# Optimization experiments

Measured on AMD Instinct MI355X. Metric: run time of the kernel, lower is better.

## Reference

```python
import jax, jax.numpy as jnp
import numpy as np

D_MODEL = 1024
NUM_HEADS = 16
HEAD_DIM = D_MODEL // NUM_HEADS


def setup_inputs() -> dict:
    key = jax.random.key(0)
    ks = jax.random.split(key, 10)
    B, SQ, SKV = 4, 2048, 2048
    s = 1.0 / np.sqrt(D_MODEL)
    return {
        "query": jax.random.normal(ks[0], (B, SQ, D_MODEL), jnp.float32),
        "key_value": jax.random.normal(ks[1], (B, SKV, D_MODEL), jnp.float32),
        "Wq": jax.random.normal(ks[2], (D_MODEL, D_MODEL), jnp.float32) * s,
        "bq": jnp.zeros((D_MODEL,), jnp.float32),
        "Wk": jax.random.normal(ks[3], (D_MODEL, D_MODEL), jnp.float32) * s,
        "bk": jnp.zeros((D_MODEL,), jnp.float32),
        "Wv": jax.random.normal(ks[4], (D_MODEL, D_MODEL), jnp.float32) * s,
        "bv": jnp.zeros((D_MODEL,), jnp.float32),
        "Wo": jax.random.normal(ks[5], (D_MODEL, D_MODEL), jnp.float32) * s,
        "bo": jnp.zeros((D_MODEL,), jnp.float32),
    }


def reference(query, key_value, Wq, bq, Wk, bk, Wv, bv, Wo, bo):
    B, SQ, _ = query.shape
    SKV = key_value.shape[1]
    H, Dh = NUM_HEADS, HEAD_DIM
    # projections (torch Linear: x @ W.T + b); split heads -> (B, H, S, Dh)
    Q = (query @ Wq.T + bq).reshape(B, SQ, H, Dh).transpose(0, 2, 1, 3)
    K = (key_value @ Wk.T + bk).reshape(B, SKV, H, Dh).transpose(0, 2, 1, 3)
    V = (key_value @ Wv.T + bv).reshape(B, SKV, H, Dh).transpose(0, 2, 1, 3)
    scale = jnp.asarray(np.sqrt(Dh), query.dtype)
    scores = jnp.einsum("bhqd,bhkd->bhqk", Q, K) / scale
    weights = jax.nn.softmax(scores, axis=-1)  # dropout is identity in eval
    attn = jnp.einsum("bhqk,bhkd->bhqd", weights, V)
    attn = attn.transpose(0, 2, 1, 3).reshape(B, SQ, H * Dh)
    return attn @ Wo.T + bo
```

## Files before the change

### kernel.cpp

```cpp
#include <hip/hip_runtime.h>

#define NH 16
#define DH 64
#define DM 1024
#define SEQ 2048
#define BATCH 4

typedef short s16x8 __attribute__((ext_vector_type(8)));
typedef float f32x4 __attribute__((ext_vector_type(4)));

__device__ __forceinline__ unsigned short f2bf(float f) {
  union { float f; unsigned int u; } v; v.f = f;
  unsigned int u = v.u;
  unsigned int r = (u + 0x7fffu + ((u >> 16) & 1u)) >> 16;
  return (unsigned short)r;
}

__device__ __forceinline__ unsigned int pkbf(float a, float b) {
#if __has_builtin(__builtin_amdgcn_cvt_pk_bf16_f32)
  typedef short v2s __attribute__((ext_vector_type(2)));
  v2s r = __builtin_amdgcn_cvt_pk_bf16_f32(a, b);
  union { v2s v; unsigned int u; } cv; cv.v = r;
  return cv.u;
#else
  return (unsigned int)f2bf(a) | ((unsigned int)f2bf(b) << 16);
#endif
}

__device__ __forceinline__ float fexp2(float x) {
#if __has_builtin(__builtin_amdgcn_exp2f)
  return __builtin_amdgcn_exp2f(x);
#else
  return exp2f(x);
#endif
}

__device__ __forceinline__ void gload_lds16(const void* g, void* l) {
  __builtin_amdgcn_global_load_lds(
      (const __attribute__((address_space(1))) unsigned int*)g,
      (__attribute__((address_space(3))) unsigned int*)l, 16, 0, 0);
}

__global__ void convert_all(const float* __restrict__ q, const float* __restrict__ kv,
                            const float* __restrict__ w0, const float* __restrict__ w1,
                            const float* __restrict__ w2, const float* __restrict__ w3,
                            unsigned short* __restrict__ oq, unsigned short* __restrict__ okv,
                            unsigned short* __restrict__ ow0, unsigned short* __restrict__ ow1,
                            unsigned short* __restrict__ ow2, unsigned short* __restrict__ ow3) {
  const int NQ4 = (BATCH * SEQ * DM) / 4;
  const int NW4 = (DM * DM) / 4;
  const int total = NQ4 * 2 + NW4 * 4;
  for (int i = blockIdx.x * blockDim.x + threadIdx.x; i < total;
       i += gridDim.x * blockDim.x) {
    const float* s; unsigned short* d; int off;
    if (i < NQ4)            { s = q;  d = oq;  off = i; }
    else if (i < 2 * NQ4)   { s = kv; d = okv; off = i - NQ4; }
    else {
      int j = i - 2 * NQ4; int wsel = j / NW4; off = j - wsel * NW4;
      s = (wsel == 0) ? w0 : (wsel == 1) ? w1 : (wsel == 2) ? w2 : w3;
      d = (wsel == 0) ? ow0 : (wsel == 1) ? ow1 : (wsel == 2) ? ow2 : ow3;
    }
    float4 v = *(const float4*)(s + (size_t)off * 4);
    ushort4 o;
    o.x = f2bf(v.x); o.y = f2bf(v.y); o.z = f2bf(v.z); o.w = f2bf(v.w);
    *(ushort4*)(d + (size_t)off * 4) = o;
  }
}

__device__ __forceinline__ void gemm_tile(const unsigned short* __restrict__ X,
                                          const unsigned short* __restrict__ Wt,
                                          unsigned short* As, unsigned short* Bs,
                                          int m0, int n0, f32x4 (*acc)[4]) {
  const int tid = threadIdx.x;
  const int wv_ = tid >> 6, lane = tid & 63;
  const int quad = lane >> 4, c = lane & 15;
  const int wm = (wv_ >> 1) * 64, wn = (wv_ & 1) * 64;
  const int srow = lane >> 3;
  const int scol = ((lane & 7) ^ srow) * 8;

  for (int kt = 0; kt < DM; kt += 64) {
#pragma unroll
    for (int i = 0; i < 4; ++i) {
      int reg = wv_ * 4 + i;
      gload_lds16(X + (size_t)(m0 + reg * 8 + srow) * DM + kt + scol,
                  (void*)(As + reg * 512));
      gload_lds16(Wt + (size_t)(n0 + reg * 8 + srow) * DM + kt + scol,
                  (void*)(Bs + reg * 512));
    }
    __syncthreads();
#pragma unroll
    for (int k2 = 0; k2 < 2; ++k2) {
      s16x8 a[4], b[4];
      int g = k2 * 4 + quad;
#pragma unroll
      for (int t = 0; t < 4; ++t)
        a[t] = *(const s16x8*)(As + (wm + t * 16 + c) * 64 + ((g ^ (c & 7)) * 8));
#pragma unroll
      for (int t = 0; t < 4; ++t)
        b[t] = *(const s16x8*)(Bs + (wn + t * 16 + c) * 64 + ((g ^ (c & 7)) * 8));
#pragma unroll
      for (int tm = 0; tm < 4; ++tm)
#pragma unroll
        for (int tn = 0; tn < 4; ++tn)
          acc[tm][tn] = __builtin_amdgcn_mfma_f32_16x16x32_bf16(
              a[tm], b[tn], acc[tm][tn], 0, 0, 0);
    }
    __syncthreads();
  }
}

__global__ __launch_bounds__(256)
void gemm_qkv(const unsigned short* __restrict__ Xq,
              const unsigned short* __restrict__ Xkv,
              const unsigned short* __restrict__ W0,
              const unsigned short* __restrict__ W1,
              const unsigned short* __restrict__ W2,
              const float* __restrict__ b0, const float* __restrict__ b1,
              const float* __restrict__ b2,
              unsigned short* __restrict__ OQ, unsigned short* __restrict__ OK_,
              unsigned short* __restrict__ OV) {
  __shared__ alignas(16) unsigned short As[128 * 64];
  __shared__ alignas(16) unsigned short Bs[128 * 64];
  const int m0 = blockIdx.x * 128;
  const int ysel = blockIdx.y >> 3;
  const int n0 = (blockIdx.y & 7) * 128;
  const unsigned short* X = (ysel == 0) ? Xq : Xkv;
  const unsigned short* Wt = (ysel == 0) ? W0 : (ysel == 1) ? W1 : W2;
  const float* bias = (ysel == 0) ? b0 : (ysel == 1) ? b1 : b2;
  unsigned short* Out = (ysel == 0) ? OQ : (ysel == 1) ? OK_ : OV;
  const float scale = (ysel == 0) ? 0.1803368801f : 1.0f;

  f32x4 acc[4][4] = {};
  gemm_tile(X, Wt, As, Bs, m0, n0, acc);

  const int tid = threadIdx.x;
  const int wv_ = tid >> 6, lane = tid & 63;
  const int quad = lane >> 4, c = lane & 15;
  const int wm = (wv_ >> 1) * 64, wn = (wv_ & 1) * 64;
#pragma unroll
  for (int tm = 0; tm < 4; ++tm) {
#pragma unroll
    for (int tn = 0; tn < 4; ++tn) {
      int n = n0 + wn + tn * 16 + c;
      float bv = bias[n];
      int m_base = m0 + wm + tm * 16 + quad * 4;
      if (ysel == 2) {
        int b_ = m_base >> 11, s_ = m_base & 2047, h_ = n >> 6, dh = n & 63;
        size_t idx = (((size_t)(b_ * NH + h_)) * DH + dh) * SEQ + s_;
        ushort4 o4;
        o4.x = f2bf(acc[tm][tn][0] + bv);
        o4.y = f2bf(acc[tm][tn][1] + bv);
        o4.z = f2bf(acc[tm][tn][2] + bv);
        o4.w = f2bf(acc[tm][tn][3] + bv);
        *(ushort4*)(&Out[idx]) = o4;
      } else {
#pragma unroll
        for (int p = 0; p < 4; ++p) {
          int m = m_base + p;
          float val = (acc[tm][tn][p] + bv) * scale;
          int b_ = m >> 11, s_ = m & 2047, h_ = n >> 6, dh = n & 63;
          size_t idx = (((size_t)(b_ * NH + h_)) * SEQ + s_) * DH + dh;
          Out[idx] = f2bf(val);
        }
      }
    }
  }
}

__global__ __launch_bounds__(256)
void gemm_o(const unsigned short* __restrict__ X,
            const unsigned short* __restrict__ Wt,
            const float* __restrict__ bias, float* __restrict__ Out) {
  __shared__ alignas(16) unsigned short As[128 * 64];
  __shared__ alignas(16) unsigned short Bs[128 * 64];
  const int m0 = blockIdx.x * 128;
  const int n0 = blockIdx.y * 128;
  f32x4 acc[4][4] = {};
  gemm_tile(X, Wt, As, Bs, m0, n0, acc);

  const int tid = threadIdx.x;
  const int wv_ = tid >> 6, lane = tid & 63;
  const int quad = lane >> 4, c = lane & 15;
  const int wm = (wv_ >> 1) * 64, wn = (wv_ & 1) * 64;
#pragma unroll
  for (int tm = 0; tm < 4; ++tm) {
#pragma unroll
    for (int tn = 0; tn < 4; ++tn) {
      int n = n0 + wn + tn * 16 + c;
      float bv = bias[n];
#pragma unroll
      for (int p = 0; p < 4; ++p) {
        int m = m0 + wm + tm * 16 + quad * 4 + p;
        Out[(size_t)m * DM + n] = acc[tm][tn][p] + bv;
      }
    }
  }
}

__global__ __launch_bounds__(256, 4)
void attn_kernel(const unsigned short* __restrict__ Qb,
                 const unsigned short* __restrict__ Kb,
                 const unsigned short* __restrict__ VTb,
                 unsigned short* __restrict__ Ob) {
  __shared__ alignas(16) unsigned short SM[16384];

  const int tid = threadIdx.x, wv_ = tid >> 6, lane = tid & 63;
  const int quad = lane >> 4, c = lane & 15;
  const int bh = blockIdx.x, qb = blockIdx.y;
  const unsigned short* Qp = Qb + (size_t)bh * SEQ * DH;
  const unsigned short* Kp = Kb + (size_t)bh * SEQ * DH;
  const unsigned short* Vp = VTb + (size_t)bh * DH * SEQ;
  const int wq0 = qb * 128 + wv_ * 32;

  s16x8 aq[2][2];
#pragma unroll
  for (int t = 0; t < 2; ++t)
#pragma unroll
    for (int k2 = 0; k2 < 2; ++k2)
      aq[t][k2] = *(const s16x8*)(Qp + (size_t)(wq0 + t * 16 + c) * DH +
                                  k2 * 32 + quad * 8);

  f32x4 ot[4][2] = {};
  float lsum[2] = {};

  const int srow = lane >> 3;
  const int schunk = (lane & 7) ^ srow;

#pragma unroll
  for (int i = 0; i < 2; ++i) {
    int reg = wv_ * 2 + i;
    gload_lds16(Kp + (size_t)(reg * 8 + srow) * DH + schunk * 8,
                (void*)(SM + reg * 512));
    gload_lds16(Vp + (size_t)(reg * 8 + srow) * SEQ + schunk * 8,
                (void*)(SM + 8192 + reg * 512));
  }

  for (int kt = 0; kt < SEQ; kt += 64) {
    const int cur = (kt >> 6) & 1;
    __syncthreads();
    if (kt + 64 < SEQ) {
      const int nxt = cur ^ 1;
#pragma unroll
      for (int i = 0; i < 2; ++i) {
        int reg = wv_ * 2 + i;
        gload_lds16(Kp + (size_t)(kt + 64 + reg * 8 + srow) * DH + schunk * 8,
                    (void*)(SM + nxt * 4096 + reg * 512));
        gload_lds16(Vp + (size_t)(reg * 8 + srow) * SEQ + kt + 64 + schunk * 8,
                    (void*)(SM + 8192 + nxt * 4096 + reg * 512));
      }
    }
    const unsigned short* K_ = SM + cur * 4096;
    const unsigned short* V_ = SM + 8192 + cur * 4096;

    f32x4 s[2][2][2] = {};
#pragma unroll
    for (int k2 = 0; k2 < 2; ++k2) {
      s16x8 ak[2][2];
#pragma unroll
      for (int jp = 0; jp < 2; ++jp)
#pragma unroll
        for (int h = 0; h < 2; ++h) {
          int r = jp * 32 + ((c >> 2) << 3) + h * 4 + (c & 3);
          int g = k2 * 4 + quad;
          ak[jp][h] = *(const s16x8*)(K_ + r * 64 + ((g ^ (r & 7)) * 8));
        }
#pragma unroll
      for (int t = 0; t < 2; ++t)
#pragma unroll
        for (int jp = 0; jp < 2; ++jp)
#pragma unroll
          for (int h = 0; h < 2; ++h)
            s[t][jp][h] = __builtin_amdgcn_mfma_f32_16x16x32_bf16(
                ak[jp][h], aq[t][k2], s[t][jp][h], 0, 0, 0);
    }

    s16x8 bp[2][2];
#pragma unroll
    for (int t = 0; t < 2; ++t)
#pragma unroll
      for (int jp = 0; jp < 2; ++jp) {
        float e00 = fexp2(s[t][jp][0][0]);
        float e01 = fexp2(s[t][jp][0][1]);
        float e02 = fexp2(s[t][jp][0][2]);
        float e03 = fexp2(s[t][jp][0][3]);
        float e10 = fexp2(s[t][jp][1][0]);
        float e11 = fexp2(s[t][jp][1][1]);
        float e12 = fexp2(s[t][jp][1][2]);
        float e13 = fexp2(s[t][jp][1][3]);
        lsum[t] += ((e00 + e01) + (e02 + e03)) + ((e10 + e11) + (e12 + e13));
        union { s16x8 v; unsigned int u[4]; } pk;
        pk.u[0] = pkbf(e00, e01);
        pk.u[1] = pkbf(e02, e03);
        pk.u[2] = pkbf(e10, e11);
        pk.u[3] = pkbf(e12, e13);
        bp[t][jp] = pk.v;
      }

#pragma unroll
    for (int jp = 0; jp < 2; ++jp)
#pragma unroll
      for (int dt = 0; dt < 4; ++dt) {
        int g = jp * 4 + quad;
        int r = dt * 16 + c;
        s16x8 av = *(const s16x8*)(V_ + r * 64 + ((g ^ (r & 7)) * 8));
#pragma unroll
        for (int t = 0; t < 2; ++t)
          ot[dt][t] = __builtin_amdgcn_mfma_f32_16x16x32_bf16(
              av, bp[t][jp], ot[dt][t], 0, 0, 0);
      }
  }

#pragma unroll
  for (int t = 0; t < 2; ++t) {
    lsum[t] += __shfl_xor(lsum[t], 16);
    lsum[t] += __shfl_xor(lsum[t], 32);
  }

  __syncthreads();

  unsigned short* Lq = SM + wv_ * (32 * 72);
#pragma unroll
  for (int t = 0; t < 2; ++t) {
    float inv = 1.0f / lsum[t];
#pragma unroll
    for (int dt = 0; dt < 4; ++dt) {
      unsigned int w01 = pkbf(ot[dt][t][0] * inv, ot[dt][t][1] * inv);
      unsigned int w23 = pkbf(ot[dt][t][2] * inv, ot[dt][t][3] * inv);
      unsigned short* p = Lq + (t * 16 + c) * 72 + dt * 16 + quad * 4;
      *(unsigned int*)(p) = w01;
      *(unsigned int*)(p + 2) = w23;
    }
  }
  const int b_ = bh >> 4, h_ = bh & 15;
  const int ql = lane >> 1, hf = lane & 1;
  const unsigned short* Lr = Lq + ql * 72 + hf * 32;
  unsigned short* Og = Ob + ((size_t)(b_ * SEQ + wq0 + ql)) * DM + h_ * 64 + hf * 32;
#pragma unroll
  for (int j = 0; j < 4; ++j) {
    s16x8 v = *(const s16x8*)(Lr + j * 8);
    *(s16x8*)(Og + j * 8) = v;
  }
}

extern "C" void kernel_launch(void* const* d_in, const int* in_sizes, int n_in,
                              void* d_out, int out_size, void* d_ws, size_t ws_size,
                              hipStream_t stream) {
  const float* q  = (const float*)d_in[0];
  const float* kv = (const float*)d_in[1];
  const float* Wq = (const float*)d_in[2];
  const float* bq = (const float*)d_in[3];
  const float* Wk = (const float*)d_in[4];
  const float* bk = (const float*)d_in[5];
  const float* Wv = (const float*)d_in[6];
  const float* bv = (const float*)d_in[7];
  const float* Wo = (const float*)d_in[8];
  const float* bo = (const float*)d_in[9];

  char* ws = (char*)d_ws;
  const size_t MB = 1024 * 1024;
  unsigned short* q_bf  = (unsigned short*)(ws);
  unsigned short* kv_bf = (unsigned short*)(ws + 16 * MB);
  unsigned short* wq_bf = (unsigned short*)(ws + 32 * MB);
  unsigned short* wk_bf = (unsigned short*)(ws + 34 * MB);
  unsigned short* wv_bf = (unsigned short*)(ws + 36 * MB);
  unsigned short* wo_bf = (unsigned short*)(ws + 38 * MB);
  unsigned short* Qb    = (unsigned short*)(ws + 40 * MB);
  unsigned short* Kb    = (unsigned short*)(ws + 56 * MB);
  unsigned short* VTb   = (unsigned short*)(ws + 72 * MB);
  unsigned short* attn  = (unsigned short*)(ws + 88 * MB);

  convert_all<<<2048, 256, 0, stream>>>(q, kv, Wq, Wk, Wv, Wo,
                                        q_bf, kv_bf, wq_bf, wk_bf, wv_bf, wo_bf);
  gemm_qkv<<<dim3(64, 24), 256, 0, stream>>>(q_bf, kv_bf, wq_bf, wk_bf, wv_bf,
                                             bq, bk, bv, Qb, Kb, VTb);
  attn_kernel<<<dim3(64, 16), 256, 0, stream>>>(Qb, Kb, VTb, attn);
  gemm_o<<<dim3(64, 8), 256, 0, stream>>>(attn, wo_bf, bo, (float*)d_out);
}
```

Baseline: 326.2 us.

## Replace projection GEMMs with 128x256 double-buffered 8-wave pipelined tiles

Rewrites the QKV and output projection GEMMs to use 512-thread blocks covering 128x256 output tiles. Global-to-LDS loads are double-buffered across K steps and interleaved with MFMA phases, using explicit vmcnt waits, raw barriers and wave priority boosts. The aim is to hide memory latency and raise operand reuse per block. In exchange it uses more LDS and halves the number of blocks, and the hand-placed waitcnt and barrier logic is fragile.

```diff
diff --git a/kernel.cpp b/kernel.cpp
--- a/kernel.cpp
+++ b/kernel.cpp
@@ -5,6 +5,7 @@
 #define DM 1024
 #define SEQ 2048
 #define BATCH 4
+#define NT 16
 
 typedef short s16x8 __attribute__((ext_vector_type(8)));
 typedef float f32x4 __attribute__((ext_vector_type(4)));
@@ -40,6 +41,8 @@
       (const __attribute__((address_space(1))) unsigned int*)g,
       (__attribute__((address_space(3))) unsigned int*)l, 16, 0, 0);
 }
+
+#define GBAR() asm volatile("s_barrier" ::: "memory")
 
 __global__ void convert_all(const float* __restrict__ q, const float* __restrict__ kv,
                             const float* __restrict__ w0, const float* __restrict__ w1,
@@ -67,63 +70,117 @@
   }
 }
 
-__device__ __forceinline__ void gemm_tile(const unsigned short* __restrict__ X,
-                                          const unsigned short* __restrict__ Wt,
-                                          unsigned short* As, unsigned short* Bs,
-                                          int m0, int n0, f32x4 (*acc)[4]) {
+template <int NJ>
+__device__ __forceinline__ void stage_rows(const unsigned short* __restrict__ src,
+                                           int row0, int kt,
+                                           unsigned short* __restrict__ dst, int tid) {
+  const int sr = tid >> 3;
+  const int g8 = ((tid & 7) ^ (sr & 7)) * 8;
+  const int wv = tid >> 6;
+#pragma unroll
+  for (int j = 0; j < NJ; ++j)
+    gload_lds16(src + (size_t)(row0 + j * 64 + sr) * DM + kt + g8,
+                dst + (j * 8 + wv) * 512);
+}
+
+__device__ __forceinline__ void gemm256_tile(const unsigned short* __restrict__ X,
+                                             const unsigned short* __restrict__ Wt,
+                                             unsigned short* __restrict__ SM,
+                                             int m0, int n0, f32x4 (*acc)[4]) {
   const int tid = threadIdx.x;
-  const int wv_ = tid >> 6, lane = tid & 63;
+  const int wv = tid >> 6, lane = tid & 63;
   const int quad = lane >> 4, c = lane & 15;
-  const int wm = (wv_ >> 1) * 64, wn = (wv_ & 1) * 64;
-  const int srow = lane >> 3;
-  const int scol = ((lane & 7) ^ srow) * 8;
-
-  for (int kt = 0; kt < DM; kt += 64) {
-#pragma unroll
-    for (int i = 0; i < 4; ++i) {
-      int reg = wv_ * 4 + i;
-      gload_lds16(X + (size_t)(m0 + reg * 8 + srow) * DM + kt + scol,
-                  (void*)(As + reg * 512));
-      gload_lds16(Wt + (size_t)(n0 + reg * 8 + srow) * DM + kt + scol,
-                  (void*)(Bs + reg * 512));
-    }
-    __syncthreads();
-#pragma unroll
-    for (int k2 = 0; k2 < 2; ++k2) {
-      s16x8 a[4], b[4];
-      int g = k2 * 4 + quad;
-#pragma unroll
-      for (int t = 0; t < 4; ++t)
-        a[t] = *(const s16x8*)(As + (wm + t * 16 + c) * 64 + ((g ^ (c & 7)) * 8));
-#pragma unroll
-      for (int t = 0; t < 4; ++t)
-        b[t] = *(const s16x8*)(Bs + (wn + t * 16 + c) * 64 + ((g ^ (c & 7)) * 8));
-#pragma unroll
-      for (int tm = 0; tm < 4; ++tm)
-#pragma unroll
-        for (int tn = 0; tn < 4; ++tn)
-          acc[tm][tn] = __builtin_amdgcn_mfma_f32_16x16x32_bf16(
-              a[tm], b[tn], acc[tm][tn], 0, 0, 0);
-    }
-    __syncthreads();
-  }
-}
-
-__global__ __launch_bounds__(256)
-void gemm_qkv(const unsigned short* __restrict__ Xq,
-              const unsigned short* __restrict__ Xkv,
-              const unsigned short* __restrict__ W0,
-              const unsigned short* __restrict__ W1,
-              const unsigned short* __restrict__ W2,
-              const float* __restrict__ b0, const float* __restrict__ b1,
-              const float* __restrict__ b2,
-              unsigned short* __restrict__ OQ, unsigned short* __restrict__ OK_,
-              unsigned short* __restrict__ OV) {
-  __shared__ alignas(16) unsigned short As[128 * 64];
-  __shared__ alignas(16) unsigned short Bs[128 * 64];
+  const int wr = wv >> 2, wc = wv & 3;
+  unsigned short* A0 = SM;
+  unsigned short* B0 = SM + 8192;
+  unsigned short* A1 = SM + 24576;
+  unsigned short* B1 = SM + 24576 + 8192;
+
+  stage_rows<2>(X, m0, 0, A0, tid);
+  stage_rows<4>(Wt, n0, 0, B0, tid);
+  stage_rows<2>(X, m0, 64, A1, tid);
+  stage_rows<4>(Wt, n0, 64, B1, tid);
+  asm volatile("s_waitcnt vmcnt(6)" ::: "memory");
+  GBAR();
+
+  const int rA0 = wr * 64 + c;
+  const int rB0 = wc * 64 + c;
+  const int c7 = c & 7;
+
+  for (int t = 0; t < NT; ++t) {
+    unsigned short* A_ = (t & 1) ? A1 : A0;
+    unsigned short* B_ = (t & 1) ? B1 : B0;
+    unsigned short* An = (t & 1) ? A0 : A1;
+
+    s16x8 af[2][2], bf[4][2];
+#pragma unroll
+    for (int fm = 0; fm < 2; ++fm)
+#pragma unroll
+      for (int k2 = 0; k2 < 2; ++k2)
+        af[fm][k2] = *(const s16x8*)(A_ + (rA0 + fm * 16) * 64 +
+                                     (((k2 * 4 + quad) ^ c7) * 8));
+#pragma unroll
+    for (int fn = 0; fn < 4; ++fn)
+#pragma unroll
+      for (int k2 = 0; k2 < 2; ++k2)
+        bf[fn][k2] = *(const s16x8*)(B_ + (rB0 + fn * 16) * 64 +
+                                     (((k2 * 4 + quad) ^ c7) * 8));
+    if (t >= 1 && t + 1 < NT)
+      stage_rows<2>(X, m0, (t + 1) * 64, An, tid);
+    GBAR();
+    __builtin_amdgcn_s_setprio(1);
+#pragma unroll
+    for (int k2 = 0; k2 < 2; ++k2)
+#pragma unroll
+      for (int fm = 0; fm < 2; ++fm)
+#pragma unroll
+        for (int fn = 0; fn < 4; ++fn)
+          acc[fm][fn] = __builtin_amdgcn_mfma_f32_16x16x32_bf16(
+              af[fm][k2], bf[fn][k2], acc[fm][fn], 0, 0, 0);
+    __builtin_amdgcn_s_setprio(0);
+    GBAR();
+
+#pragma unroll
+    for (int fm = 0; fm < 2; ++fm)
+#pragma unroll
+      for (int k2 = 0; k2 < 2; ++k2)
+        af[fm][k2] = *(const s16x8*)(A_ + (rA0 + (fm + 2) * 16) * 64 +
+                                     (((k2 * 4 + quad) ^ c7) * 8));
+    if (t + 2 < NT) {
+      stage_rows<4>(Wt, n0, (t + 2) * 64, B_, tid);
+      asm volatile("s_waitcnt vmcnt(4)" ::: "memory");
+    } else {
+      asm volatile("s_waitcnt vmcnt(0)" ::: "memory");
+    }
+    GBAR();
+    __builtin_amdgcn_s_setprio(1);
+#pragma unroll
+    for (int k2 = 0; k2 < 2; ++k2)
+#pragma unroll
+      for (int fm = 0; fm < 2; ++fm)
+#pragma unroll
+        for (int fn = 0; fn < 4; ++fn)
+          acc[fm + 2][fn] = __builtin_amdgcn_mfma_f32_16x16x32_bf16(
+              af[fm][k2], bf[fn][k2], acc[fm + 2][fn], 0, 0, 0);
+    __builtin_amdgcn_s_setprio(0);
+    GBAR();
+  }
+}
+
+__global__ __launch_bounds__(512, 2)
+void gemm_qkv256(const unsigned short* __restrict__ Xq,
+                 const unsigned short* __restrict__ Xkv,
+                 const unsigned short* __restrict__ W0,
+                 const unsigned short* __restrict__ W1,
+                 const unsigned short* __restrict__ W2,
+                 const float* __restrict__ b0, const float* __restrict__ b1,
+                 const float* __restrict__ b2,
+                 unsigned short* __restrict__ OQ, unsigned short* __restrict__ OK_,
+                 unsigned short* __restrict__ OV) {
+  __shared__ alignas(16) unsigned short SM[49152];
   const int m0 = blockIdx.x * 128;
-  const int ysel = blockIdx.y >> 3;
-  const int n0 = (blockIdx.y & 7) * 128;
+  const int ysel = blockIdx.y >> 2;
+  const int n0 = (blockIdx.y & 3) * 256;
   const unsigned short* X = (ysel == 0) ? Xq : Xkv;
   const unsigned short* Wt = (ysel == 0) ? W0 : (ysel == 1) ? W1 : W2;
   const float* bias = (ysel == 0) ? b0 : (ysel == 1) ? b1 : b2;
@@ -131,33 +188,35 @@
   const float scale = (ysel == 0) ? 0.1803368801f : 1.0f;
 
   f32x4 acc[4][4] = {};
-  gemm_tile(X, Wt, As, Bs, m0, n0, acc);
+  gemm256_tile(X, Wt, SM, m0, n0, acc);
 
   const int tid = threadIdx.x;
-  const int wv_ = tid >> 6, lane = tid & 63;
+  const int wv = tid >> 6, lane = tid & 63;
   const int quad = lane >> 4, c = lane & 15;
-  const int wm = (wv_ >> 1) * 64, wn = (wv_ & 1) * 64;
-#pragma unroll
-  for (int tm = 0; tm < 4; ++tm) {
-#pragma unroll
-    for (int tn = 0; tn < 4; ++tn) {
-      int n = n0 + wn + tn * 16 + c;
+  const int wr = wv >> 2, wc = wv & 3;
+  const int m0w = m0 + wr * 64;
+  const int n0w = n0 + wc * 64;
+#pragma unroll
+  for (int fm = 0; fm < 4; ++fm) {
+#pragma unroll
+    for (int fn = 0; fn < 4; ++fn) {
+      int n = n0w + fn * 16 + c;
       float bv = bias[n];
-      int m_base = m0 + wm + tm * 16 + quad * 4;
+      int m_base = m0w + fm * 16 + quad * 4;
       if (ysel == 2) {
         int b_ = m_base >> 11, s_ = m_base & 2047, h_ = n >> 6, dh = n & 63;
         size_t idx = (((size_t)(b_ * NH + h_)) * DH + dh) * SEQ + s_;
         ushort4 o4;
-        o4.x = f2bf(acc[tm][tn][0] + bv);
-        o4.y = f2bf(acc[tm][tn][1] + bv);
-        o4.z = f2bf(acc[tm][tn][2] + bv);
-        o4.w = f2bf(acc[tm][tn][3] + bv);
+        o4.x = f2bf(acc[fm][fn][0] + bv);
+        o4.y = f2bf(acc[fm][fn][1] + bv);
+        o4.z = f2bf(acc[fm][fn][2] + bv);
+        o4.w = f2bf(acc[fm][fn][3] + bv);
         *(ushort4*)(&Out[idx]) = o4;
       } else {
 #pragma unroll
         for (int p = 0; p < 4; ++p) {
           int m = m_base + p;
-          float val = (acc[tm][tn][p] + bv) * scale;
+          float val = (acc[fm][fn][p] + bv) * scale;
           int b_ = m >> 11, s_ = m & 2047, h_ = n >> 6, dh = n & 63;
           size_t idx = (((size_t)(b_ * NH + h_)) * SEQ + s_) * DH + dh;
           Out[idx] = f2bf(val);
@@ -167,31 +226,32 @@
   }
 }
 
-__global__ __launch_bounds__(256)
-void gemm_o(const unsigned short* __restrict__ X,
-            const unsigned short* __restrict__ Wt,
-            const float* __restrict__ bias, float* __restrict__ Out) {
-  __shared__ alignas(16) unsigned short As[128 * 64];
-  __shared__ alignas(16) unsigned short Bs[128 * 64];
+__global__ __launch_bounds__(512, 2)
+void gemm_o256(const unsigned short* __restrict__ X,
+               const unsigned short* __restrict__ Wt,
+               const float* __restrict__ bias, float* __restrict__ Out) {
+  __shared__ alignas(16) unsigned short SM[49152];
   const int m0 = blockIdx.x * 128;
-  const int n0 = blockIdx.y * 128;
+  const int n0 = blockIdx.y * 256;
   f32x4 acc[4][4] = {};
-  gemm_tile(X, Wt, As, Bs, m0, n0, acc);
+  gemm256_tile(X, Wt, SM, m0, n0, acc);
 
   const int tid = threadIdx.x;
-  const int wv_ = tid >> 6, lane = tid & 63;
+  const int wv = tid >> 6, lane = tid & 63;
   const int quad = lane >> 4, c = lane & 15;
-  const int wm = (wv_ >> 1) * 64, wn = (wv_ & 1) * 64;
-#pragma unroll
-  for (int tm = 0; tm < 4; ++tm) {
-#pragma unroll
-    for (int tn = 0; tn < 4; ++tn) {
-      int n = n0 + wn + tn * 16 + c;
+  const int wr = wv >> 2, wc = wv & 3;
+  const int m0w = m0 + wr * 64;
+  const int n0w = n0 + wc * 64;
+#pragma unroll
+  for (int fm = 0; fm < 4; ++fm) {
+#pragma unroll
+    for (int fn = 0; fn < 4; ++fn) {
+      int n = n0w + fn * 16 + c;
       float bv = bias[n];
 #pragma unroll
       for (int p = 0; p < 4; ++p) {
-        int m = m0 + wm + tm * 16 + quad * 4 + p;
-        Out[(size_t)m * DM + n] = acc[tm][tn][p] + bv;
+        int m = m0w + fm * 16 + quad * 4 + p;
+        Out[(size_t)m * DM + n] = acc[fm][fn][p] + bv;
       }
     }
   }
@@ -371,8 +431,8 @@
 
   convert_all<<<2048, 256, 0, stream>>>(q, kv, Wq, Wk, Wv, Wo,
                                         q_bf, kv_bf, wq_bf, wk_bf, wv_bf, wo_bf);
-  gemm_qkv<<<dim3(64, 24), 256, 0, stream>>>(q_bf, kv_bf, wq_bf, wk_bf, wv_bf,
-                                             bq, bk, bv, Qb, Kb, VTb);
+  gemm_qkv256<<<dim3(64, 12), 512, 0, stream>>>(q_bf, kv_bf, wq_bf, wk_bf, wv_bf,
+                                                bq, bk, bv, Qb, Kb, VTb);
   attn_kernel<<<dim3(64, 16), 256, 0, stream>>>(Qb, Kb, VTb, attn);
-  gemm_o<<<dim3(64, 8), 256, 0, stream>>>(attn, wo_bf, bo, (float*)d_out);
-}
+  gemm_o256<<<dim3(64, 4), 512, 0, stream>>>(attn, wo_bf, bo, (float*)d_out);
+}
```

Measured after the change: 328.3 us. Within noise of the previous version (+0.7%).
